# Kernel optimization log

Hardware: AMD Instinct MI355X
Metric: run time of the kernel (lower is better)

## Reference

```python
import jax, jax.numpy as jnp
import numpy as np

LN2 = 0.69314718  # matches the 2ln2 constant in the original rbf()


def setup_inputs() -> dict:
    key = jax.random.key(0)
    domain_min = [-1.0, -1.0, -1.0]
    domain_max = [1.0, 1.0, 1.0]
    n = [12, 12, 12]
    codomain_dim = 128
    N = 200000

    axes = [jnp.linspace(domain_min[i], domain_max[i], n[i], dtype=jnp.float32)
            for i in range(len(n))]
    # torch.meshgrid default is 'ij' indexing
    grid = jnp.stack(jnp.meshgrid(*axes, indexing='ij'), axis=-1).reshape(-1, len(n))  # [G, 3]

    # rbf_width: mean nearest-neighbor distance on the grid (second-smallest per row)
    d = jnp.linalg.norm(grid[:, None, :] - grid[None, :, :], axis=-1)  # [G, G], G=1728 -> small
    width = jnp.sort(d, axis=1)[:, 1].mean()

    # interpolation matrix m and coeffs = solve(m, weight), as in __init__ (no_grad buffer)
    m = jnp.exp(-(d ** 2) / (width ** 2 / LN2))
    k1, k2 = jax.random.split(key)
    weight = jax.random.normal(k1, (grid.shape[0], codomain_dim), dtype=jnp.float32)
    coeffs = jnp.linalg.solve(m, weight)  # [G, C]

    x = jax.random.normal(k2, (N, len(n)), dtype=jnp.float32)  # [N, 3]
    return {"x": x, "grid": grid, "coeffs": coeffs, "width": width}


def reference(x, grid, coeffs, width):
    # Squared Euclidean distance via |a|^2 + |b|^2 - 2ab (avoids [N, G, 3] broadcast tensor).
    # rbf(d, w) = exp(-d^2 / (w^2 / ln2)); since it only uses d^2, skip the sqrt.
    x2 = jnp.sum(x * x, axis=-1, keepdims=True)          # [N, 1]
    g2 = jnp.sum(grid * grid, axis=-1)                   # [G]
    d2 = x2 + g2[None, :] - 2.0 * (x @ grid.T)           # [N, G]
    d2 = jnp.maximum(d2, 0.0)                            # numerical guard
    p = jnp.exp(-d2 * (LN2 / (width * width)))           # [N, G]
    return p @ coeffs                                    # [N, C]
```

## Files before the change

kernel.cpp:

```cpp
#include <hip/hip_runtime.h>
#include <stdint.h>


typedef _Float16 f16;
typedef _Float16 f16x8 __attribute__((ext_vector_type(8)));
typedef float f32x16 __attribute__((ext_vector_type(16)));

#define LN2F 0.69314718f
#define LOG2E 1.4426950408889634f

#define CD 128
#define KD 1728

__global__ void prep_coeffs(const float* __restrict__ coeffs,
                            f16* __restrict__ img) {
  int kp  = blockIdx.x * 2 + (threadIdx.x >> 7);
  int col = threadIdx.x & 127;
  int i   = kp / 144;
  int r   = kp - i * 144;
  int s   = r >> 4;
  int idx = r & 15;
  int hh  = idx >> 3;
  int b   = idx & 7;
  int j, k2;
  if (s < 6) { j = 2 * s + hh;                 k2 = b; }
  else       { j = 4 * (s - 6) + 2 * hh + (b >> 2); k2 = 8 + (b & 3); }
  float v = coeffs[(size_t)((i * 12 + j) * 12 + k2) * CD + col];
  f16 h = (f16)v;
  f16 l = (f16)(v - (float)h);
  int q   = i * 9 + s;
  int ch2 = col >> 6;
  int c64 = col & 63;
  size_t o = (size_t)q * 4096 + ch2 * 2048 + hh * 512 + c64 * 8 + b;
  img[o]        = h;
  img[o + 1024] = l;
}

union FU { uint32_t u[4]; f16x8 v; };

__global__ __launch_bounds__(256) void rbf_gemm(
    const float* __restrict__ x,
    const float* __restrict__ width,
    const f16* __restrict__ img,
    float* __restrict__ out, int N) {
  const int t    = threadIdx.x;
  const int lane = t & 63;
  const int wv   = t >> 6;
  const int l31  = lane & 31;
  const int hh   = lane >> 5;
  const int rbase = blockIdx.x * 128;
  const int ch2   = blockIdx.y;

  const float w  = width[0];
  const float s2 = (LN2F * LOG2E) / (w * w);

  int rr = rbase + wv * 32 + l31;
  if (rr >= N) rr = N - 1;
  const float x0 = x[(size_t)rr * 3 + 0];
  const float x1 = x[(size_t)rr * 3 + 1];
  const float x2 = x[(size_t)rr * 3 + 2];

  float e1a[12], e2a[12];
#pragma unroll
  for (int k = 0; k < 12; ++k) {
    float g  = (float)k * (2.0f / 11.0f) - 1.0f;
    float d1 = x1 - g;
    float d2 = x2 - g;
    e1a[k] = __builtin_amdgcn_exp2f(-d1 * d1 * s2);
    e2a[k] = __builtin_amdgcn_exp2f(-d2 * d2 * s2);
  }

  const int voff = ch2 * 4096 + hh * 1024 + l31 * 16;
  const char* imgb = (const char*)img;

  f16x8 cb0 = *(const f16x8*)(imgb + voff + 0);
  f16x8 cb1 = *(const f16x8*)(imgb + voff + 512);
  f16x8 cb2 = *(const f16x8*)(imgb + voff + 2048);
  f16x8 cb3 = *(const f16x8*)(imgb + voff + 2560);

  f32x16 acc0, acc1;
#pragma unroll
  for (int q = 0; q < 16; ++q) { acc0[q] = 0.f; acc1[q] = 0.f; }

#pragma unroll 1
  for (int i = 0; i < 12; ++i) {
    float gi  = (float)i * (2.0f / 11.0f) - 1.0f;
    float d0  = x0 - gi;
    float e0i = __builtin_amdgcn_exp2f(-d0 * d0 * s2);

#pragma unroll
    for (int s = 0; s < 9; ++s) {
      const char* spn = imgb + (size_t)(i * 9 + s + 1) * 8192;
      f16x8 nb0 = *(const f16x8*)(spn + voff + 0);
      f16x8 nb1 = *(const f16x8*)(spn + voff + 512);
      f16x8 nb2 = *(const f16x8*)(spn + voff + 2048);
      f16x8 nb3 = *(const f16x8*)(spn + voff + 2560);

      FU ah, al;
      if (s < 6) {
        float es = e0i * (hh ? e1a[2 * s + 1] : e1a[2 * s]);
#pragma unroll
        for (int q = 0; q < 4; ++q) {
          float ea = e2a[2 * q];
          float eb = e2a[2 * q + 1];
          uint32_t hq, lq;
          asm("v_fma_mixlo_f16 %0, %1, %2, 0"
              : "=v"(hq) : "v"(es), "v"(ea));
          asm("v_fma_mixhi_f16 %0, %1, %2, 0"
              : "+v"(hq) : "v"(es), "v"(eb));
          asm("v_fma_mixlo_f16 %0, %1, %2, -%3 op_sel:[0,0,0] op_sel_hi:[0,0,1]"
              : "=v"(lq) : "v"(es), "v"(ea), "v"(hq));
          asm("v_fma_mixhi_f16 %0, %1, %2, -%3 op_sel:[0,0,1] op_sel_hi:[0,0,1]"
              : "+v"(lq) : "v"(es), "v"(eb), "v"(hq));
          ah.u[q] = hq;
          al.u[q] = lq;
        }
      } else {
        int J0 = 4 * (s - 6);
        float c01 = e0i * (hh ? e1a[J0 + 2] : e1a[J0 + 0]);
        float c23 = e0i * (hh ? e1a[J0 + 3] : e1a[J0 + 1]);
#pragma unroll
        for (int q = 0; q < 4; ++q) {
          float es = (q < 2) ? c01 : c23;
          float ea = e2a[8 + 2 * (q & 1)];
          float eb = e2a[9 + 2 * (q & 1)];
          uint32_t hq, lq;
          asm("v_fma_mixlo_f16 %0, %1, %2, 0"
              : "=v"(hq) : "v"(es), "v"(ea));
          asm("v_fma_mixhi_f16 %0, %1, %2, 0"
              : "+v"(hq) : "v"(es), "v"(eb));
          asm("v_fma_mixlo_f16 %0, %1, %2, -%3 op_sel:[0,0,0] op_sel_hi:[0,0,1]"
              : "=v"(lq) : "v"(es), "v"(ea), "v"(hq));
          asm("v_fma_mixhi_f16 %0, %1, %2, -%3 op_sel:[0,0,1] op_sel_hi:[0,0,1]"
              : "+v"(lq) : "v"(es), "v"(eb), "v"(hq));
          ah.u[q] = hq;
          al.u[q] = lq;
        }
      }

      acc0 = __builtin_amdgcn_mfma_f32_32x32x16_f16(ah.v, cb0, acc0, 0, 0, 0);
      acc1 = __builtin_amdgcn_mfma_f32_32x32x16_f16(ah.v, cb1, acc1, 0, 0, 0);
      acc0 = __builtin_amdgcn_mfma_f32_32x32x16_f16(al.v, cb0, acc0, 0, 0, 0);
      acc1 = __builtin_amdgcn_mfma_f32_32x32x16_f16(al.v, cb1, acc1, 0, 0, 0);
      acc0 = __builtin_amdgcn_mfma_f32_32x32x16_f16(ah.v, cb2, acc0, 0, 0, 0);
      acc1 = __builtin_amdgcn_mfma_f32_32x32x16_f16(ah.v, cb3, acc1, 0, 0, 0);

      cb0 = nb0; cb1 = nb1; cb2 = nb2; cb3 = nb3;
    }
  }

#pragma unroll
  for (int q = 0; q < 16; ++q) {
    int row = rbase + wv * 32 + (q & 3) + 8 * (q >> 2) + 4 * hh;
    if (row < N) {
      int col = ch2 * 64 + l31;
      out[(size_t)row * CD + col]      = acc0[q];
      out[(size_t)row * CD + col + 32] = acc1[q];
    }
  }
}

__global__ void rbf_fallback(const float* __restrict__ x, const float* __restrict__ grid,
                             const float* __restrict__ coeffs, const float* __restrict__ width,
                             float* __restrict__ out, int N) {
  int row = blockIdx.x;
  int col = threadIdx.x;
  if (row >= N) return;
  float x0 = x[(size_t)row * 3 + 0];
  float x1 = x[(size_t)row * 3 + 1];
  float x2 = x[(size_t)row * 3 + 2];
  float w = width[0];
  float s2 = (LN2F * LOG2E) / (w * w);
  float acc = 0.f;
  for (int g = 0; g < 1728; ++g) {
    float d0 = x0 - grid[g * 3 + 0];
    float d1 = x1 - grid[g * 3 + 1];
    float d2 = x2 - grid[g * 3 + 2];
    float p = exp2f(-(d0 * d0 + d1 * d1 + d2 * d2) * s2);
    acc += p * coeffs[(size_t)g * CD + col];
  }
  out[(size_t)row * CD + col] = acc;
}

extern "C" void kernel_launch(void* const* d_in, const int* in_sizes, int n_in,
                              void* d_out, int out_size, void* d_ws, size_t ws_size,
                              hipStream_t stream) {
  const float* x      = (const float*)d_in[0];
  const float* grid   = (const float*)d_in[1];
  const float* coeffs = (const float*)d_in[2];
  const float* width  = (const float*)d_in[3];
  float* out = (float*)d_out;
  int N = in_sizes[0] / 3;

  size_t need = (size_t)KD * CD * 2 * sizeof(f16) + 16384;
  if (ws_size >= need) {
    f16* img = (f16*)d_ws;
    hipLaunchKernelGGL(prep_coeffs, dim3(KD / 2), dim3(256), 0, stream,
                       coeffs, img);
    int nb = (N + 127) / 128;
    hipLaunchKernelGGL(rbf_gemm, dim3(nb, 2), dim3(256), 0, stream,
                       x, width, img, out, N);
  } else {
    hipLaunchKernelGGL(rbf_fallback, dim3(N), dim3(CD), 0, stream,
                       x, grid, coeffs, width, out, N);
  }
}
```

Before: 264.5 us.

## Give each wave two 32-row tiles to reuse coefficient fragments across MFMAs

Each wave now computes 64 rows as two 32-row M tiles that share the same loaded coefficient B fragments. This halves global/L2 coefficient loads per output and gives more independent MFMA chains to hide latency. Prefetch depth goes from one step to two, and the MFMA block is wrapped in s_setprio. Blocks shrink to 128 threads, and each wave holds four accumulators, which raises register pressure and may lower occupancy.

Result: faster. 246.1 us (-7.0%).

```diff
diff --git a/kernel.cpp b/kernel.cpp
--- a/kernel.cpp
+++ b/kernel.cpp
@@ -38,7 +38,7 @@
 
 union FU { uint32_t u[4]; f16x8 v; };
 
-__global__ __launch_bounds__(256) void rbf_gemm(
+__global__ __launch_bounds__(128) void rbf_gemm(
     const float* __restrict__ x,
     const float* __restrict__ width,
     const f16* __restrict__ img,
@@ -54,20 +54,24 @@
   const float w  = width[0];
   const float s2 = (LN2F * LOG2E) / (w * w);
 
-  int rr = rbase + wv * 32 + l31;
-  if (rr >= N) rr = N - 1;
-  const float x0 = x[(size_t)rr * 3 + 0];
-  const float x1 = x[(size_t)rr * 3 + 1];
-  const float x2 = x[(size_t)rr * 3 + 2];
-
-  float e1a[12], e2a[12];
+  int r0 = rbase + wv * 64 + l31;      if (r0 >= N) r0 = N - 1;
+  int r1 = rbase + wv * 64 + 32 + l31; if (r1 >= N) r1 = N - 1;
+  const float x00 = x[(size_t)r0 * 3 + 0];
+  const float x01 = x[(size_t)r0 * 3 + 1];
+  const float x02 = x[(size_t)r0 * 3 + 2];
+  const float x10 = x[(size_t)r1 * 3 + 0];
+  const float x11 = x[(size_t)r1 * 3 + 1];
+  const float x12 = x[(size_t)r1 * 3 + 2];
+
+  float e1a[2][12], e2a[2][12];
 #pragma unroll
   for (int k = 0; k < 12; ++k) {
-    float g  = (float)k * (2.0f / 11.0f) - 1.0f;
-    float d1 = x1 - g;
-    float d2 = x2 - g;
-    e1a[k] = __builtin_amdgcn_exp2f(-d1 * d1 * s2);
-    e2a[k] = __builtin_amdgcn_exp2f(-d2 * d2 * s2);
+    float g = (float)k * (2.0f / 11.0f) - 1.0f;
+    float d;
+    d = x01 - g; e1a[0][k] = __builtin_amdgcn_exp2f(-d * d * s2);
+    d = x11 - g; e1a[1][k] = __builtin_amdgcn_exp2f(-d * d * s2);
+    d = x02 - g; e2a[0][k] = __builtin_amdgcn_exp2f(-d * d * s2);
+    d = x12 - g; e2a[1][k] = __builtin_amdgcn_exp2f(-d * d * s2);
   }
 
   const int voff = ch2 * 4096 + hh * 1024 + l31 * 16;
@@ -77,85 +81,110 @@
   f16x8 cb1 = *(const f16x8*)(imgb + voff + 512);
   f16x8 cb2 = *(const f16x8*)(imgb + voff + 2048);
   f16x8 cb3 = *(const f16x8*)(imgb + voff + 2560);
-
-  f32x16 acc0, acc1;
-#pragma unroll
-  for (int q = 0; q < 16; ++q) { acc0[q] = 0.f; acc1[q] = 0.f; }
+  f16x8 db0 = *(const f16x8*)(imgb + 8192 + voff + 0);
+  f16x8 db1 = *(const f16x8*)(imgb + 8192 + voff + 512);
+  f16x8 db2 = *(const f16x8*)(imgb + 8192 + voff + 2048);
+  f16x8 db3 = *(const f16x8*)(imgb + 8192 + voff + 2560);
+
+  f32x16 acc00, acc01, acc10, acc11;
+#pragma unroll
+  for (int q = 0; q < 16; ++q) { acc00[q] = 0.f; acc01[q] = 0.f; acc10[q] = 0.f; acc11[q] = 0.f; }
 
 #pragma unroll 1
   for (int i = 0; i < 12; ++i) {
-    float gi  = (float)i * (2.0f / 11.0f) - 1.0f;
-    float d0  = x0 - gi;
-    float e0i = __builtin_amdgcn_exp2f(-d0 * d0 * s2);
+    float gi = (float)i * (2.0f / 11.0f) - 1.0f;
+    float d0;
+    d0 = x00 - gi; float e00 = __builtin_amdgcn_exp2f(-d0 * d0 * s2);
+    d0 = x10 - gi; float e01v = __builtin_amdgcn_exp2f(-d0 * d0 * s2);
 
 #pragma unroll
     for (int s = 0; s < 9; ++s) {
-      const char* spn = imgb + (size_t)(i * 9 + s + 1) * 8192;
+      const char* spn = imgb + (size_t)(i * 9 + s + 2) * 8192;
       f16x8 nb0 = *(const f16x8*)(spn + voff + 0);
       f16x8 nb1 = *(const f16x8*)(spn + voff + 512);
       f16x8 nb2 = *(const f16x8*)(spn + voff + 2048);
       f16x8 nb3 = *(const f16x8*)(spn + voff + 2560);
 
-      FU ah, al;
-      if (s < 6) {
-        float es = e0i * (hh ? e1a[2 * s + 1] : e1a[2 * s]);
-#pragma unroll
-        for (int q = 0; q < 4; ++q) {
-          float ea = e2a[2 * q];
-          float eb = e2a[2 * q + 1];
-          uint32_t hq, lq;
-          asm("v_fma_mixlo_f16 %0, %1, %2, 0"
-              : "=v"(hq) : "v"(es), "v"(ea));
-          asm("v_fma_mixhi_f16 %0, %1, %2, 0"
-              : "+v"(hq) : "v"(es), "v"(eb));
-          asm("v_fma_mixlo_f16 %0, %1, %2, -%3 op_sel:[0,0,0] op_sel_hi:[0,0,1]"
-              : "=v"(lq) : "v"(es), "v"(ea), "v"(hq));
-          asm("v_fma_mixhi_f16 %0, %1, %2, -%3 op_sel:[0,0,1] op_sel_hi:[0,0,1]"
-              : "+v"(lq) : "v"(es), "v"(eb), "v"(hq));
-          ah.u[q] = hq;
-          al.u[q] = lq;
-        }
-      } else {
-        int J0 = 4 * (s - 6);
-        float c01 = e0i * (hh ? e1a[J0 + 2] : e1a[J0 + 0]);
-        float c23 = e0i * (hh ? e1a[J0 + 3] : e1a[J0 + 1]);
-#pragma unroll
-        for (int q = 0; q < 4; ++q) {
-          float es = (q < 2) ? c01 : c23;
-          float ea = e2a[8 + 2 * (q & 1)];
-          float eb = e2a[9 + 2 * (q & 1)];
-          uint32_t hq, lq;
-          asm("v_fma_mixlo_f16 %0, %1, %2, 0"
-              : "=v"(hq) : "v"(es), "v"(ea));
-          asm("v_fma_mixhi_f16 %0, %1, %2, 0"
-              : "+v"(hq) : "v"(es), "v"(eb));
-          asm("v_fma_mixlo_f16 %0, %1, %2, -%3 op_sel:[0,0,0] op_sel_hi:[0,0,1]"
-              : "=v"(lq) : "v"(es), "v"(ea), "v"(hq));
-          asm("v_fma_mixhi_f16 %0, %1, %2, -%3 op_sel:[0,0,1] op_sel_hi:[0,0,1]"
-              : "+v"(lq) : "v"(es), "v"(eb), "v"(hq));
-          ah.u[q] = hq;
-          al.u[q] = lq;
+      FU ah0, al0, ah1, al1;
+#pragma unroll
+      for (int mi = 0; mi < 2; ++mi) {
+        float e0i = mi ? e01v : e00;
+        FU* pah = mi ? &ah1 : &ah0;
+        FU* pal = mi ? &al1 : &al0;
+        if (s < 6) {
+          float es = e0i * (hh ? e1a[mi][2 * s + 1] : e1a[mi][2 * s]);
+#pragma unroll
+          for (int q = 0; q < 4; ++q) {
+            float ea = e2a[mi][2 * q];
+            float eb = e2a[mi][2 * q + 1];
+            uint32_t hq, lq;
+            asm("v_fma_mixlo_f16 %0, %1, %2, 0"
+                : "=v"(hq) : "v"(es), "v"(ea));
+            asm("v_fma_mixhi_f16 %0, %1, %2, 0"
+                : "+v"(hq) : "v"(es), "v"(eb));
+            asm("v_fma_mixlo_f16 %0, %1, %2, -%3 op_sel:[0,0,0] op_sel_hi:[0,0,1]"
+                : "=v"(lq) : "v"(es), "v"(ea), "v"(hq));
+            asm("v_fma_mixhi_f16 %0, %1, %2, -%3 op_sel:[0,0,1] op_sel_hi:[0,0,1]"
+                : "+v"(lq) : "v"(es), "v"(eb), "v"(hq));
+            pah->u[q] = hq;
+            pal->u[q] = lq;
+          }
+        } else {
+          int J0 = 4 * (s - 6);
+          float c01 = e0i * (hh ? e1a[mi][J0 + 2] : e1a[mi][J0 + 0]);
+          float c23 = e0i * (hh ? e1a[mi][J0 + 3] : e1a[mi][J0 + 1]);
+#pragma unroll
+          for (int q = 0; q < 4; ++q) {
+            float es = (q < 2) ? c01 : c23;
+            float ea = e2a[mi][8 + 2 * (q & 1)];
+            float eb = e2a[mi][9 + 2 * (q & 1)];
+            uint32_t hq, lq;
+            asm("v_fma_mixlo_f16 %0, %1, %2, 0"
+                : "=v"(hq) : "v"(es), "v"(ea));
+            asm("v_fma_mixhi_f16 %0, %1, %2, 0"
+                : "+v"(hq) : "v"(es), "v"(eb));
+            asm("v_fma_mixlo_f16 %0, %1, %2, -%3 op_sel:[0,0,0] op_sel_hi:[0,0,1]"
+                : "=v"(lq) : "v"(es), "v"(ea), "v"(hq));
+            asm("v_fma_mixhi_f16 %0, %1, %2, -%3 op_sel:[0,0,1] op_sel_hi:[0,0,1]"
+                : "+v"(lq) : "v"(es), "v"(eb), "v"(hq));
+            pah->u[q] = hq;
+            pal->u[q] = lq;
+          }
         }
       }
 
-      acc0 = __builtin_amdgcn_mfma_f32_32x32x16_f16(ah.v, cb0, acc0, 0, 0, 0);
-      acc1 = __builtin_amdgcn_mfma_f32_32x32x16_f16(ah.v, cb1, acc1, 0, 0, 0);
-      acc0 = __builtin_amdgcn_mfma_f32_32x32x16_f16(al.v, cb0, acc0, 0, 0, 0);
-      acc1 = __builtin_amdgcn_mfma_f32_32x32x16_f16(al.v, cb1, acc1, 0, 0, 0);
-      acc0 = __builtin_amdgcn_mfma_f32_32x32x16_f16(ah.v, cb2, acc0, 0, 0, 0);
-      acc1 = __builtin_amdgcn_mfma_f32_32x32x16_f16(ah.v, cb3, acc1, 0, 0, 0);
-
-      cb0 = nb0; cb1 = nb1; cb2 = nb2; cb3 = nb3;
+      __builtin_amdgcn_s_setprio(1);
+      acc00 = __builtin_amdgcn_mfma_f32_32x32x16_f16(ah0.v, cb0, acc00, 0, 0, 0);
+      acc01 = __builtin_amdgcn_mfma_f32_32x32x16_f16(ah0.v, cb1, acc01, 0, 0, 0);
+      acc10 = __builtin_amdgcn_mfma_f32_32x32x16_f16(ah1.v, cb0, acc10, 0, 0, 0);
+      acc11 = __builtin_amdgcn_mfma_f32_32x32x16_f16(ah1.v, cb1, acc11, 0, 0, 0);
+      acc00 = __builtin_amdgcn_mfma_f32_32x32x16_f16(al0.v, cb0, acc00, 0, 0, 0);
+      acc01 = __builtin_amdgcn_mfma_f32_32x32x16_f16(al0.v, cb1, acc01, 0, 0, 0);
+      acc10 = __builtin_amdgcn_mfma_f32_32x32x16_f16(al1.v, cb0, acc10, 0, 0, 0);
+      acc11 = __builtin_amdgcn_mfma_f32_32x32x16_f16(al1.v, cb1, acc11, 0, 0, 0);
+      acc00 = __builtin_amdgcn_mfma_f32_32x32x16_f16(ah0.v, cb2, acc00, 0, 0, 0);
+      acc01 = __builtin_amdgcn_mfma_f32_32x32x16_f16(ah0.v, cb3, acc01, 0, 0, 0);
+      acc10 = __builtin_amdgcn_mfma_f32_32x32x16_f16(ah1.v, cb2, acc10, 0, 0, 0);
+      acc11 = __builtin_amdgcn_mfma_f32_32x32x16_f16(ah1.v, cb3, acc11, 0, 0, 0);
+      __builtin_amdgcn_s_setprio(0);
+
+      cb0 = db0; cb1 = db1; cb2 = db2; cb3 = db3;
+      db0 = nb0; db1 = nb1; db2 = nb2; db3 = nb3;
     }
   }
 
 #pragma unroll
   for (int q = 0; q < 16; ++q) {
-    int row = rbase + wv * 32 + (q & 3) + 8 * (q >> 2) + 4 * hh;
-    if (row < N) {
-      int col = ch2 * 64 + l31;
-      out[(size_t)row * CD + col]      = acc0[q];
-      out[(size_t)row * CD + col + 32] = acc1[q];
+    int row0 = rbase + wv * 64 + (q & 3) + 8 * (q >> 2) + 4 * hh;
+    int col  = ch2 * 64 + l31;
+    if (row0 < N) {
+      out[(size_t)row0 * CD + col]      = acc00[q];
+      out[(size_t)row0 * CD + col + 32] = acc01[q];
+    }
+    int row1 = row0 + 32;
+    if (row1 < N) {
+      out[(size_t)row1 * CD + col]      = acc10[q];
+      out[(size_t)row1 * CD + col + 32] = acc11[q];
     }
   }
 }
@@ -192,13 +221,13 @@
   float* out = (float*)d_out;
   int N = in_sizes[0] / 3;
 
-  size_t need = (size_t)KD * CD * 2 * sizeof(f16) + 16384;
+  size_t need = (size_t)108 * 8192 + 2 * 8192;
   if (ws_size >= need) {
     f16* img = (f16*)d_ws;
     hipLaunchKernelGGL(prep_coeffs, dim3(KD / 2), dim3(256), 0, stream,
                        coeffs, img);
     int nb = (N + 127) / 128;
-    hipLaunchKernelGGL(rbf_gemm, dim3(nb, 2), dim3(256), 0, stream,
+    hipLaunchKernelGGL(rbf_gemm, dim3(nb, 2), dim3(128), 0, stream,
                        x, width, img, out, N);
   } else {
     hipLaunchKernelGGL(rbf_fallback, dim3(N), dim3(CD), 0, stream,
```
